# Kernel optimization log

Hardware: AMD Instinct MI355X
Metric: run time of the kernel (lower is better)

The kernel has to match this reference:

```python
import jax, jax.numpy as jnp
import numpy as np

C = 64
C2 = C // 2

def setup_inputs() -> dict:
    key = jax.random.key(0)
    ks = jax.random.split(key, 5)
    x = jax.random.normal(ks[0], (8, C, 64, 64), dtype=jnp.float32)
    # 1x1 conv weights stored as [out, in] matrices (kernel size 1)
    g_w = jax.random.normal(ks[1], (C2, C), dtype=jnp.float32) * (1.0 / np.sqrt(C))
    g_b = jax.random.normal(ks[2], (C2,), dtype=jnp.float32) * 0.01
    W_w = jax.random.normal(ks[3], (C, C2), dtype=jnp.float32) * (1.0 / np.sqrt(C2))
    W_b = jax.random.normal(ks[4], (C,), dtype=jnp.float32) * 0.01
    return {"x": x, "g_w": g_w, "g_b": g_b, "W_w": W_w, "W_b": W_b}

def reference(x, g_w, g_b, W_w, W_b):
    b, c, h, w = x.shape
    xf = x.reshape(b, c, h * w)                      # [B, C, N]
    # g: 1x1 conv -> [B, N, C2]
    g_x = jnp.einsum('oc,bcn->bno', g_w, xf) + g_b
    # attention scores on raw x (theta/phi convs unused in original forward)
    f = jnp.einsum('bcn,bcm->bnm', xf, xf)           # [B, N, N]
    f_div_C = jax.nn.softmax(f, axis=-1)
    y = jnp.einsum('bnm,bmo->bno', f_div_C, g_x)     # [B, N, C2]
    # W: 1x1 conv back to C channels, then residual
    W_y = jnp.einsum('co,bno->bcn', W_w, y) + W_b[None, :, None]
    z = W_y.reshape(b, c, h, w) + x
    return z
```

## Files before the change

kernel.cpp:

```cpp
#include <hip/hip_runtime.h>
#include <hip/hip_bf16.h>

#define BATCH 8
#define CH    64
#define CH2   32
#define NN    4096
#define BN    (BATCH * NN)
#define KPAD  72
#define VPAD  72
#define YPAD  36
#define RPAD  40
#define MAXSPLIT 8

typedef __attribute__((ext_vector_type(8)))  short        short8;
typedef __attribute__((ext_vector_type(4)))  float        floatx4;
typedef __attribute__((ext_vector_type(16))) float        floatx16;
typedef __attribute__((ext_vector_type(4)))  unsigned int uint4v;
typedef __attribute__((ext_vector_type(8)))  unsigned short ushort8v;
typedef unsigned short ushort_t;

#define LOG2E      1.4426950408889634f
#define SQRT_LOG2E 1.2011224087864498f

__device__ __forceinline__ unsigned short f2bf_rne(float f) {
    unsigned int u = __float_as_uint(f);
    return (unsigned short)((u + 0x7FFFu + ((u >> 16) & 1u)) >> 16);
}

__global__ __launch_bounds__(256) void prep_fused(const float* __restrict__ x,
                                                  const float* __restrict__ gw,
                                                  const float* __restrict__ gb,
                                                  ushort_t* __restrict__ xT,
                                                  float* __restrict__ mlog,
                                                  ushort_t* __restrict__ gxT) {
    __shared__ float gwl[CH2 * CH];
    __shared__ float gbl[CH2];
    int t = threadIdx.x;
    for (int i = t; i < CH2 * CH; i += 256) gwl[i] = gw[i];
    if (t < CH2) gbl[t] = gb[t];
    __syncthreads();

    int g   = blockIdx.x * 256 + t;
    int row = g >> 2;
    int q4  = g & 3;
    int b = row >> 12, n = row & (NN - 1);
    const float* xp = x + (size_t)b * CH * NN + n;

    float xv[16];
    #pragma unroll
    for (int j = 0; j < 16; ++j) xv[j] = xp[(size_t)(q4 * 16 + j) * NN];

    float ns = 0.f;
    short8 v0, v1;
    #pragma unroll
    for (int j = 0; j < 8; ++j) {
        ns += xv[j] * xv[j];
        v0[j] = (short)f2bf_rne(xv[j] * SQRT_LOG2E);
    }
    #pragma unroll
    for (int j = 0; j < 8; ++j) {
        ns += xv[8 + j] * xv[8 + j];
        v1[j] = (short)f2bf_rne(xv[8 + j] * SQRT_LOG2E);
    }
    *(short8*)(xT + (size_t)row * CH + q4 * 16)     = v0;
    *(short8*)(xT + (size_t)row * CH + q4 * 16 + 8) = v1;
    ns += __shfl_xor(ns, 1);
    ns += __shfl_xor(ns, 2);
    if (q4 == 0) mlog[row] = 12.0f * sqrtf(ns) * LOG2E;

    float acc[CH2];
    #pragma unroll
    for (int o = 0; o < CH2; ++o) {
        const float4* wr = (const float4*)(gwl + o * CH + q4 * 16);
        float4 w0 = wr[0], w1 = wr[1], w2 = wr[2], w3 = wr[3];
        float a;
        a  = w0.x * xv[0]  + w0.y * xv[1]  + w0.z * xv[2]  + w0.w * xv[3];
        a += w1.x * xv[4]  + w1.y * xv[5]  + w1.z * xv[6]  + w1.w * xv[7];
        a += w2.x * xv[8]  + w2.y * xv[9]  + w2.z * xv[10] + w2.w * xv[11];
        a += w3.x * xv[12] + w3.y * xv[13] + w3.z * xv[14] + w3.w * xv[15];
        acc[o] = a;
    }
    #pragma unroll
    for (int o = 0; o < CH2; ++o) {
        acc[o] += __shfl_xor(acc[o], 1);
        acc[o] += __shfl_xor(acc[o], 2);
    }
    #pragma unroll
    for (int i = 0; i < 8; ++i) {
        int o = q4 * 8 + i;
        gxT[((size_t)b * CH2 + o) * NN + n] = f2bf_rne(acc[o] + gbl[o]);
    }
}

__global__ __launch_bounds__(256, 4) void flash_attn(const ushort_t* __restrict__ xT,
                                                     const ushort_t* __restrict__ gxT,
                                                     const float* __restrict__ mlog,
                                                     ushort_t* __restrict__ py,
                                                     float* __restrict__ pl,
                                                     int ksplit) {
    __shared__ __align__(16) unsigned char smem[18432];
    ushort_t* Klds = (ushort_t*)smem;
    ushort_t* Vlds = Klds + 64 * KPAD;

    const int tid = threadIdx.x, wave = tid >> 6, lane = tid & 63;
    const int q5 = lane & 31;
    const int h  = lane >> 5;
    const int bq = blockIdx.x & 255;
    const int sp = blockIdx.x >> 8;
    const int b = bq >> 5, qt = bq & 31;
    const int n0 = qt * 128 + wave * 32;
    const int k0 = sp * ksplit;

    short8 qf[4];
    {
        const ushort_t* qp = xT + ((size_t)(b * NN + n0 + q5)) * CH + h * 8;
        #pragma unroll
        for (int f = 0; f < 4; ++f) qf[f] = *(const short8*)(qp + f * 16);
    }
    const float ml = mlog[(size_t)b * NN + n0 + q5];

    floatx16 mlC;
    #pragma unroll
    for (int i = 0; i < 16; ++i) mlC[i] = -ml;

    floatx16 yt;
    #pragma unroll
    for (int i = 0; i < 16; ++i) yt[i] = 0.f;
    float lsum = 0.f;

    const ushort_t* kb = xT + (size_t)(b * NN + k0) * CH;
    const ushort_t* vb = gxT + (size_t)b * CH2 * NN + k0;
    const int iters = ksplit >> 6;
    const int skey = tid >> 3, sc0 = (tid & 7) * 8;

    for (int kt = 0; kt < iters; ++kt) {
        const size_t kof = (size_t)kt << 12;
        short8 gk0 = *(const short8*)(kb + kof + (size_t)skey * CH + sc0);
        short8 gk1 = *(const short8*)(kb + kof + (size_t)(skey + 32) * CH + sc0);
        short8 gv  = *(const short8*)(vb + (size_t)skey * NN + kt * 64 + sc0);

        __syncthreads();
        *(short8*)(&Klds[skey * KPAD + sc0])        = gk0;
        *(short8*)(&Klds[(skey + 32) * KPAD + sc0]) = gk1;
        *(short8*)(&Vlds[skey * VPAD + sc0])        = gv;
        __syncthreads();

        short8 vf[4];
        #pragma unroll
        for (int fr = 0; fr < 4; ++fr)
            vf[fr] = *(const short8*)(&Vlds[q5 * VPAD + fr * 16 + h * 8]);

        #pragma unroll
        for (int T = 0; T < 2; ++T) {
            floatx16 st;
            __builtin_amdgcn_s_setprio(1);
            {
                short8 kf = *(const short8*)(&Klds[(T * 32 + q5) * KPAD + h * 8]);
                st = __builtin_amdgcn_mfma_f32_32x32x16_bf16(kf, qf[0], mlC, 0, 0, 0);
            }
            #pragma unroll
            for (int f = 1; f < 4; ++f) {
                short8 kf = *(const short8*)(&Klds[(T * 32 + q5) * KPAD + f * 16 + h * 8]);
                st = __builtin_amdgcn_mfma_f32_32x32x16_bf16(kf, qf[f], st, 0, 0, 0);
            }
            __builtin_amdgcn_s_setprio(0);
            unsigned int d[8];
            #pragma unroll
            for (int r2 = 0; r2 < 8; ++r2) {
                float p0 = __builtin_amdgcn_exp2f(st[2 * r2]);
                float p1 = __builtin_amdgcn_exp2f(st[2 * r2 + 1]);
                lsum += p0;
                lsum += p1;
                unsigned int pk;
                asm("v_cvt_pk_bf16_f32 %0, %1, %2" : "=v"(pk) : "v"(p0), "v"(p1));
                d[r2] = pk;
            }
            #pragma unroll
            for (int fp = 0; fp < 2; ++fp) {
                unsigned int b0 = d[fp * 4 + 0], b1 = d[fp * 4 + 1];
                unsigned int b2 = d[fp * 4 + 2], b3 = d[fp * 4 + 3];
                asm("v_permlane32_swap_b32 %0, %1" : "+v"(b0), "+v"(b2));
                asm("v_permlane32_swap_b32 %0, %1" : "+v"(b1), "+v"(b3));
                uint4v bv;
                bv[0] = b0; bv[1] = b1; bv[2] = b2; bv[3] = b3;
                short8 pb = __builtin_bit_cast(short8, bv);
                __builtin_amdgcn_s_setprio(1);
                yt = __builtin_amdgcn_mfma_f32_32x32x16_bf16(vf[T * 2 + fp], pb, yt, 0, 0, 0);
                __builtin_amdgcn_s_setprio(0);
            }
        }
    }

    lsum += __shfl_xor(lsum, 32);

    __syncthreads();
    float* yb = (float*)smem + wave * 32 * YPAD;
    #pragma unroll
    for (int reg = 0; reg < 16; ++reg) {
        int o = (reg & 3) + 8 * (reg >> 2) + 4 * h;
        yb[q5 * YPAD + o] = yt[reg];
    }
    __syncthreads();
    {
        int qq = lane >> 1, half = lane & 1;
        const float* src = yb + qq * YPAD + half * 16;
        float4 s0 = *(const float4*)(src);
        float4 s1 = *(const float4*)(src + 4);
        float4 s2 = *(const float4*)(src + 8);
        float4 s3 = *(const float4*)(src + 12);
        ushort8v pk0, pk1;
        pk0[0] = f2bf_rne(s0.x); pk0[1] = f2bf_rne(s0.y);
        pk0[2] = f2bf_rne(s0.z); pk0[3] = f2bf_rne(s0.w);
        pk0[4] = f2bf_rne(s1.x); pk0[5] = f2bf_rne(s1.y);
        pk0[6] = f2bf_rne(s1.z); pk0[7] = f2bf_rne(s1.w);
        pk1[0] = f2bf_rne(s2.x); pk1[1] = f2bf_rne(s2.y);
        pk1[2] = f2bf_rne(s2.z); pk1[3] = f2bf_rne(s2.w);
        pk1[4] = f2bf_rne(s3.x); pk1[5] = f2bf_rne(s3.y);
        pk1[6] = f2bf_rne(s3.z); pk1[7] = f2bf_rne(s3.w);
        ushort_t* dst = py + ((size_t)sp * BN + (size_t)b * NN + n0 + qq) * CH2 + half * 16;
        *(ushort8v*)(dst)     = pk0;
        *(ushort8v*)(dst + 8) = pk1;
    }
    if (h == 0) pl[(size_t)sp * BN + (size_t)b * NN + n0 + q5] = lsum;
}

__global__ __launch_bounds__(256) void reduce_proj(const ushort_t* __restrict__ py,
                                                   const float* __restrict__ pl,
                                                   const float* __restrict__ Ww,
                                                   const float* __restrict__ Wb,
                                                   const float* __restrict__ x,
                                                   float* __restrict__ out,
                                                   int nsplit) {
    __shared__ ushort_t WwB[CH * RPAD];
    __shared__ ushort_t Y[64 * RPAD];
    __shared__ float    linv[64];
    __shared__ float    WbL[CH];

    const int t = threadIdx.x;
    const int row = t >> 2, o8 = (t & 3) * 8;
    const int grow0 = blockIdx.x * 64;

    {
        const float* wp = Ww + row * CH2 + o8;
        ushort8v w;
        #pragma unroll
        for (int j = 0; j < 8; ++j) w[j] = f2bf_rne(wp[j]);
        *(ushort8v*)(&WwB[row * RPAD + o8]) = w;
    }
    if (t < CH) WbL[t] = Wb[t];
    if (t < 64) {
        const float* plp = pl + grow0 + t;
        float lv[MAXSPLIT];
        #pragma unroll
        for (int s = 0; s < MAXSPLIT; ++s) {
            int sc = s < nsplit ? s : 0;
            lv[s] = plp[(size_t)sc * BN];
        }
        float l = 0.f;
        #pragma unroll
        for (int s = 0; s < MAXSPLIT; ++s) if (s < nsplit) l += lv[s];
        linv[t] = 1.0f / l;
    }

    float acc[8];
    #pragma unroll
    for (int j = 0; j < 8; ++j) acc[j] = 0.f;
    {
        const ushort_t* pp = py + ((size_t)(grow0 + row)) * CH2 + o8;
        ushort8v pv[MAXSPLIT];
        #pragma unroll
        for (int s = 0; s < MAXSPLIT; ++s) {
            int sc = s < nsplit ? s : 0;
            pv[s] = *(const ushort8v*)(pp + (size_t)sc * BN * CH2);
        }
        #pragma unroll
        for (int s = 0; s < MAXSPLIT; ++s) if (s < nsplit) {
            #pragma unroll
            for (int j = 0; j < 8; ++j)
                acc[j] += __uint_as_float((unsigned int)pv[s][j] << 16);
        }
    }
    __syncthreads();
    {
        float inv = linv[row];
        ushort8v yv;
        #pragma unroll
        for (int j = 0; j < 8; ++j) yv[j] = f2bf_rne(acc[j] * inv);
        *(ushort8v*)(&Y[row * RPAD + o8]) = yv;
    }
    __syncthreads();

    const int wave = t >> 6, lane = t & 63;
    const int ql = lane & 15, quad = lane >> 4;
    const int b = grow0 >> 12;
    const int nbase = (grow0 & (NN - 1)) + wave * 16;

    short8 bfrag = *(const short8*)(&Y[(wave * 16 + ql) * RPAD + quad * 8]);
    #pragma unroll
    for (int ct = 0; ct < 4; ++ct) {
        short8 afrag = *(const short8*)(&WwB[(ct * 16 + ql) * RPAD + quad * 8]);
        floatx4 d = (floatx4){0.f, 0.f, 0.f, 0.f};
        d = __builtin_amdgcn_mfma_f32_16x16x32_bf16(afrag, bfrag, d, 0, 0, 0);
        #pragma unroll
        for (int r = 0; r < 4; ++r) {
            int c = ct * 16 + quad * 4 + r;
            size_t oi = ((size_t)b * CH + c) * NN + nbase + ql;
            out[oi] = d[r] + WbL[c] + x[oi];
        }
    }
}

extern "C" void kernel_launch(void* const* d_in, const int* in_sizes, int n_in,
                              void* d_out, int out_size, void* d_ws, size_t ws_size,
                              hipStream_t stream) {
    const float* x  = (const float*)d_in[0];
    const float* gw = (const float*)d_in[1];
    const float* gb = (const float*)d_in[2];
    const float* Ww = (const float*)d_in[3];
    const float* Wb = (const float*)d_in[4];
    float* out = (float*)d_out;

    ushort_t* xT   = (ushort_t*)d_ws;
    ushort_t* gxT  = xT + (size_t)BN * CH;
    float*    mlog = (float*)(gxT + (size_t)BATCH * CH2 * NN);
    ushort_t* py   = (ushort_t*)(mlog + BN);
    size_t base_bytes = (size_t)BN * CH * 2 + (size_t)BATCH * CH2 * NN * 2 + (size_t)BN * 4;
    int split = MAXSPLIT;
    while (split > 1 && base_bytes + (size_t)split * BN * (CH2 * 2 + 4) > ws_size)
        split >>= 1;
    float* pl = (float*)(py + (size_t)split * BN * CH2);

    hipLaunchKernelGGL(prep_fused,  dim3(BN * 4 / 256), dim3(256), 0, stream,
                       x, gw, gb, xT, mlog, gxT);
    hipLaunchKernelGGL(flash_attn,  dim3(256 * split),  dim3(256), 0, stream,
                       xT, gxT, mlog, py, pl, NN / split);
    hipLaunchKernelGGL(reduce_proj, dim3(BN / 64),      dim3(256), 0, stream,
                       py, pl, Ww, Wb, x, out, split);
}
```

Measured before the change: 112.0 us.

## Store K/V in MFMA fragment layout and load directly from global, dropping LDS staging

The prep kernel now writes the bf16 x and g(x) tensors in a pre-swizzled layout that matches the MFMA operand fragments. The attention kernel then loads each lane's K and V fragments straight from global memory with contiguous 16-byte loads, removing the LDS staging and both per-tile barriers. The softmax max offset moves from the MFMA accumulator init into a subtraction before exp2, and the row sum is split into two accumulators. In exchange, every wave independently re-reads K/V from global or L2 instead of sharing a block-wide LDS copy, and the explicit setprio hints are removed.

New measurement: 118.8 us. 1.06x slower.

```diff
diff --git a/kernel.cpp b/kernel.cpp
--- a/kernel.cpp
+++ b/kernel.cpp
@@ -6,8 +6,6 @@
 #define CH2   32
 #define NN    4096
 #define BN    (BATCH * NN)
-#define KPAD  72
-#define VPAD  72
 #define YPAD  36
 #define RPAD  40
 #define MAXSPLIT 8
@@ -27,12 +25,13 @@
     return (unsigned short)((u + 0x7FFFu + ((u >> 16) & 1u)) >> 16);
 }
 
+
 __global__ __launch_bounds__(256) void prep_fused(const float* __restrict__ x,
                                                   const float* __restrict__ gw,
                                                   const float* __restrict__ gb,
-                                                  ushort_t* __restrict__ xT,
+                                                  ushort_t* __restrict__ xF,
                                                   float* __restrict__ mlog,
-                                                  ushort_t* __restrict__ gxT) {
+                                                  ushort_t* __restrict__ gxF) {
     __shared__ float gwl[CH2 * CH];
     __shared__ float gbl[CH2];
     int t = threadIdx.x;
@@ -62,8 +61,11 @@
         ns += xv[8 + j] * xv[8 + j];
         v1[j] = (short)f2bf_rne(xv[8 + j] * SQRT_LOG2E);
     }
-    *(short8*)(xT + (size_t)row * CH + q4 * 16)     = v0;
-    *(short8*)(xT + (size_t)row * CH + q4 * 16 + 8) = v1;
+    {
+        size_t pb8 = (((size_t)b * 128 + (n >> 5)) * 4 + q4) * 2;
+        *(short8*)(xF + pb8 * 256 + (size_t)(n & 31) * 8)       = v0;
+        *(short8*)(xF + (pb8 + 1) * 256 + (size_t)(n & 31) * 8) = v1;
+    }
     ns += __shfl_xor(ns, 1);
     ns += __shfl_xor(ns, 2);
     if (q4 == 0) mlog[row] = 12.0f * sqrtf(ns) * LOG2E;
@@ -85,22 +87,23 @@
         acc[o] += __shfl_xor(acc[o], 1);
         acc[o] += __shfl_xor(acc[o], 2);
     }
-    #pragma unroll
-    for (int i = 0; i < 8; ++i) {
-        int o = q4 * 8 + i;
-        gxT[((size_t)b * CH2 + o) * NN + n] = f2bf_rne(acc[o] + gbl[o]);
-    }
-}
-
-__global__ __launch_bounds__(256, 4) void flash_attn(const ushort_t* __restrict__ xT,
-                                                     const ushort_t* __restrict__ gxT,
+    {
+        size_t vbase = (((size_t)b * 256 + (n >> 4)) * 2 + ((n >> 3) & 1)) * 256 + (n & 7);
+        #pragma unroll
+        for (int i = 0; i < 8; ++i) {
+            int o = q4 * 8 + i;
+            gxF[vbase + (size_t)o * 8] = f2bf_rne(acc[o] + gbl[o]);
+        }
+    }
+}
+
+__global__ __launch_bounds__(256, 4) void flash_attn(const ushort_t* __restrict__ xF,
+                                                     const ushort_t* __restrict__ gxF,
                                                      const float* __restrict__ mlog,
                                                      ushort_t* __restrict__ py,
                                                      float* __restrict__ pl,
                                                      int ksplit) {
     __shared__ __align__(16) unsigned char smem[18432];
-    ushort_t* Klds = (ushort_t*)smem;
-    ushort_t* Vlds = Klds + 64 * KPAD;
 
     const int tid = threadIdx.x, wave = tid >> 6, lane = tid & 63;
     const int q5 = lane & 31;
@@ -113,87 +116,72 @@
 
     short8 qf[4];
     {
-        const ushort_t* qp = xT + ((size_t)(b * NN + n0 + q5)) * CH + h * 8;
-        #pragma unroll
-        for (int f = 0; f < 4; ++f) qf[f] = *(const short8*)(qp + f * 16);
+        const ushort_t* qp = xF + ((((size_t)b * 128 + qt * 4 + wave) * 4) * 2 + h) * 256 + q5 * 8;
+        #pragma unroll
+        for (int f = 0; f < 4; ++f) qf[f] = *(const short8*)(qp + f * 512);
     }
     const float ml = mlog[(size_t)b * NN + n0 + q5];
 
-    floatx16 mlC;
-    #pragma unroll
-    for (int i = 0; i < 16; ++i) mlC[i] = -ml;
-
     floatx16 yt;
     #pragma unroll
     for (int i = 0; i < 16; ++i) yt[i] = 0.f;
-    float lsum = 0.f;
-
-    const ushort_t* kb = xT + (size_t)(b * NN + k0) * CH;
-    const ushort_t* vb = gxT + (size_t)b * CH2 * NN + k0;
-    const int iters = ksplit >> 6;
-    const int skey = tid >> 3, sc0 = (tid & 7) * 8;
-
-    for (int kt = 0; kt < iters; ++kt) {
-        const size_t kof = (size_t)kt << 12;
-        short8 gk0 = *(const short8*)(kb + kof + (size_t)skey * CH + sc0);
-        short8 gk1 = *(const short8*)(kb + kof + (size_t)(skey + 32) * CH + sc0);
-        short8 gv  = *(const short8*)(vb + (size_t)skey * NN + kt * 64 + sc0);
-
-        __syncthreads();
-        *(short8*)(&Klds[skey * KPAD + sc0])        = gk0;
-        *(short8*)(&Klds[(skey + 32) * KPAD + sc0]) = gk1;
-        *(short8*)(&Vlds[skey * VPAD + sc0])        = gv;
-        __syncthreads();
-
-        short8 vf[4];
-        #pragma unroll
-        for (int fr = 0; fr < 4; ++fr)
-            vf[fr] = *(const short8*)(&Vlds[q5 * VPAD + fr * 16 + h * 8]);
-
-        #pragma unroll
-        for (int T = 0; T < 2; ++T) {
-            floatx16 st;
-            __builtin_amdgcn_s_setprio(1);
+    float ls0 = 0.f, ls1 = 0.f;
+
+    const int nsub = ksplit >> 5;
+    const ushort_t* kp = xF + ((((size_t)b * 128 + (k0 >> 5)) * 4) * 2 + h) * 256 + q5 * 8;
+    const ushort_t* vp = gxF + (((size_t)b * 256 + (k0 >> 4)) * 2 + h) * 256 + q5 * 8;
+
+    for (int s = 0; s < nsub; ++s) {
+        const ushort_t* kps = kp + (size_t)s * 2048;
+        short8 kf0 = *(const short8*)(kps);
+        short8 kf1 = *(const short8*)(kps + 512);
+        short8 kf2 = *(const short8*)(kps + 1024);
+        short8 kf3 = *(const short8*)(kps + 1536);
+        short8 vf0 = *(const short8*)(vp + (size_t)(s * 2) * 512);
+        short8 vf1 = *(const short8*)(vp + (size_t)(s * 2 + 1) * 512);
+
+        floatx16 st;
+        #pragma unroll
+        for (int i = 0; i < 16; ++i) st[i] = 0.f;
+        st = __builtin_amdgcn_mfma_f32_32x32x16_bf16(kf0, qf[0], st, 0, 0, 0);
+        st = __builtin_amdgcn_mfma_f32_32x32x16_bf16(kf1, qf[1], st, 0, 0, 0);
+        st = __builtin_amdgcn_mfma_f32_32x32x16_bf16(kf2, qf[2], st, 0, 0, 0);
+        st = __builtin_amdgcn_mfma_f32_32x32x16_bf16(kf3, qf[3], st, 0, 0, 0);
+
+        #pragma unroll
+        for (int fp = 0; fp < 2; ++fp) {
+            unsigned int d0, d1, d2, d3;
             {
-                short8 kf = *(const short8*)(&Klds[(T * 32 + q5) * KPAD + h * 8]);
-                st = __builtin_amdgcn_mfma_f32_32x32x16_bf16(kf, qf[0], mlC, 0, 0, 0);
+                float p0 = __builtin_amdgcn_exp2f(st[fp * 8 + 0] - ml);
+                float p1 = __builtin_amdgcn_exp2f(st[fp * 8 + 1] - ml);
+                float p2 = __builtin_amdgcn_exp2f(st[fp * 8 + 2] - ml);
+                float p3 = __builtin_amdgcn_exp2f(st[fp * 8 + 3] - ml);
+                float p4 = __builtin_amdgcn_exp2f(st[fp * 8 + 4] - ml);
+                float p5 = __builtin_amdgcn_exp2f(st[fp * 8 + 5] - ml);
+                float p6 = __builtin_amdgcn_exp2f(st[fp * 8 + 6] - ml);
+                float p7 = __builtin_amdgcn_exp2f(st[fp * 8 + 7] - ml);
+                ls0 += p0 + p2;
+                ls1 += p1 + p3;
+                ls0 += p4 + p6;
+                ls1 += p5 + p7;
+                asm("v_cvt_pk_bf16_f32 %0, %1, %2" : "=v"(d0) : "v"(p0), "v"(p1));
+                asm("v_cvt_pk_bf16_f32 %0, %1, %2" : "=v"(d1) : "v"(p2), "v"(p3));
+                asm("v_cvt_pk_bf16_f32 %0, %1, %2" : "=v"(d2) : "v"(p4), "v"(p5));
+                asm("v_cvt_pk_bf16_f32 %0, %1, %2" : "=v"(d3) : "v"(p6), "v"(p7));
             }
-            #pragma unroll
-            for (int f = 1; f < 4; ++f) {
-                short8 kf = *(const short8*)(&Klds[(T * 32 + q5) * KPAD + f * 16 + h * 8]);
-                st = __builtin_amdgcn_mfma_f32_32x32x16_bf16(kf, qf[f], st, 0, 0, 0);
-            }
-            __builtin_amdgcn_s_setprio(0);
-            unsigned int d[8];
-            #pragma unroll
-            for (int r2 = 0; r2 < 8; ++r2) {
-                float p0 = __builtin_amdgcn_exp2f(st[2 * r2]);
-                float p1 = __builtin_amdgcn_exp2f(st[2 * r2 + 1]);
-                lsum += p0;
-                lsum += p1;
-                unsigned int pk;
-                asm("v_cvt_pk_bf16_f32 %0, %1, %2" : "=v"(pk) : "v"(p0), "v"(p1));
-                d[r2] = pk;
-            }
-            #pragma unroll
-            for (int fp = 0; fp < 2; ++fp) {
-                unsigned int b0 = d[fp * 4 + 0], b1 = d[fp * 4 + 1];
-                unsigned int b2 = d[fp * 4 + 2], b3 = d[fp * 4 + 3];
-                asm("v_permlane32_swap_b32 %0, %1" : "+v"(b0), "+v"(b2));
-                asm("v_permlane32_swap_b32 %0, %1" : "+v"(b1), "+v"(b3));
-                uint4v bv;
-                bv[0] = b0; bv[1] = b1; bv[2] = b2; bv[3] = b3;
-                short8 pb = __builtin_bit_cast(short8, bv);
-                __builtin_amdgcn_s_setprio(1);
-                yt = __builtin_amdgcn_mfma_f32_32x32x16_bf16(vf[T * 2 + fp], pb, yt, 0, 0, 0);
-                __builtin_amdgcn_s_setprio(0);
-            }
-        }
-    }
-
+            asm("v_permlane32_swap_b32 %0, %1" : "+v"(d0), "+v"(d2));
+            asm("v_permlane32_swap_b32 %0, %1" : "+v"(d1), "+v"(d3));
+            uint4v bv;
+            bv[0] = d0; bv[1] = d1; bv[2] = d2; bv[3] = d3;
+            short8 pb = __builtin_bit_cast(short8, bv);
+            short8 vf = fp ? vf1 : vf0;
+            yt = __builtin_amdgcn_mfma_f32_32x32x16_bf16(vf, pb, yt, 0, 0, 0);
+        }
+    }
+
+    float lsum = ls0 + ls1;
     lsum += __shfl_xor(lsum, 32);
 
-    __syncthreads();
     float* yb = (float*)smem + wave * 32 * YPAD;
     #pragma unroll
     for (int reg = 0; reg < 16; ++reg) {
@@ -320,9 +308,9 @@
     const float* Wb = (const float*)d_in[4];
     float* out = (float*)d_out;
 
-    ushort_t* xT   = (ushort_t*)d_ws;
-    ushort_t* gxT  = xT + (size_t)BN * CH;
-    float*    mlog = (float*)(gxT + (size_t)BATCH * CH2 * NN);
+    ushort_t* xF   = (ushort_t*)d_ws;
+    ushort_t* gxF  = xF + (size_t)BN * CH;
+    float*    mlog = (float*)(gxF + (size_t)BATCH * CH2 * NN);
     ushort_t* py   = (ushort_t*)(mlog + BN);
     size_t base_bytes = (size_t)BN * CH * 2 + (size_t)BATCH * CH2 * NN * 2 + (size_t)BN * 4;
     int split = MAXSPLIT;
@@ -331,9 +319,9 @@
     float* pl = (float*)(py + (size_t)split * BN * CH2);
 
     hipLaunchKernelGGL(prep_fused,  dim3(BN * 4 / 256), dim3(256), 0, stream,
-                       x, gw, gb, xT, mlog, gxT);
+                       x, gw, gb, xF, mlog, gxF);
     hipLaunchKernelGGL(flash_attn,  dim3(256 * split),  dim3(256), 0, stream,
-                       xT, gxT, mlog, py, pl, NN / split);
+                       xF, gxF, mlog, py, pl, NN / split);
     hipLaunchKernelGGL(reduce_proj, dim3(BN / 64),      dim3(256), 0, stream,
                        py, pl, Ww, Wb, x, out, split);
 }
```
